# Performance work log

Hardware: AMD Instinct MI355X
Metric: run time of the kernel (lower is better)

## Reference

```python
import jax, jax.numpy as jnp
import numpy as np

N = 100_000   # nodes per type
E = 800_000   # edges per relation
H = 128       # hidden_channels
O = 64        # out_channels
TIME_SCALE = 1.0
LN_EPS = 1e-5


def setup_inputs() -> dict:
    key = jax.random.key(0)
    ks = jax.random.split(key, 24)
    nrm = lambda k, shp, s=1.0: jax.random.normal(k, shp, jnp.float32) * s
    inp = {}
    inp["x_A"] = nrm(ks[0], (N, H))
    inp["x_B"] = nrm(ks[1], (N, H))
    inp["x_C"] = nrm(ks[2], (N, H))
    inp["t_A"] = jax.random.uniform(ks[3], (N,), jnp.float32) * 1000.0
    inp["t_B"] = jax.random.uniform(ks[4], (N,), jnp.float32) * 1000.0
    inp["t_C"] = jax.random.uniform(ks[5], (N,), jnp.float32) * 1000.0
    inp["edge1"] = jnp.stack([jax.random.randint(ks[6], (E,), 0, N),
                              jax.random.randint(ks[7], (E,), 0, N)]).astype(jnp.int32)
    inp["edge2"] = jnp.stack([jax.random.randint(ks[8], (E,), 0, N),
                              jax.random.randint(ks[9], (E,), 0, N)]).astype(jnp.int32)
    kk = 10
    for i in range(2):
        inp[f"Wl{i}"] = nrm(ks[kk], (H, H), 0.05); kk += 1
        inp[f"bl{i}"] = jnp.zeros((H,), jnp.float32)
        inp[f"W0{i}"] = nrm(ks[kk], (H, H), 0.05); kk += 1
        inp[f"b0{i}"] = jnp.zeros((H,), jnp.float32)
        inp[f"W1{i}"] = nrm(ks[kk], (H, H), 0.05); kk += 1
        inp[f"b1{i}"] = jnp.zeros((H,), jnp.float32)
        inp[f"gate{i}"] = jnp.asarray(0.5, jnp.float32)
        inp[f"lam{i}"] = jnp.asarray(0.1, jnp.float32)  # raw lambda
        inp[f"lng{i}"] = jnp.ones((H,), jnp.float32)
        inp[f"lnb{i}"] = jnp.zeros((H,), jnp.float32)
    inp["Wout"] = nrm(ks[kk], (H, O), 0.05)
    inp["bout"] = jnp.zeros((O,), jnp.float32)
    return inp


def _layer(h_src, h_dst, x0_dst, edge, t_src, t_dst,
           Wl, bl, W0, b0, W1, b1, gate, raw_lam, lng, lnb):
    s, d = edge[0], edge[1]
    n_dst = h_dst.shape[0]
    # per-edge time-decay weight
    lam = jax.nn.softplus(raw_lam) + 1e-8
    delta = jnp.maximum((t_dst[d] - t_src[s]) / TIME_SCALE, 0.0)
    w = jnp.exp(jnp.maximum(-lam * delta, -60.0))          # [E]
    # gather + weight + scatter-add  (propagate with aggr='add')
    msg = h_src[s] * w[:, None]                            # [E,H]
    agg = jax.ops.segment_sum(msg, d, num_segments=n_dst)  # [n_dst,H]
    deg = jnp.maximum(jax.ops.segment_sum(w, d, num_segments=n_dst), 1e-6)
    out = agg / deg[:, None]
    g = jax.nn.sigmoid(gate)
    y = out @ Wl + bl + (1.0 - g) * (h_dst @ W0 + b0) + g * (x0_dst @ W1 + b1)
    y = jax.nn.relu(y)
    mu = jnp.mean(y, axis=-1, keepdims=True)
    var = jnp.mean((y - mu) ** 2, axis=-1, keepdims=True)
    y = (y - mu) * jax.lax.rsqrt(var + LN_EPS) * lng + lnb
    # index_copy_: only nodes that appear as a destination get updated
    cnt = jax.ops.segment_sum(jnp.ones_like(w), d, num_segments=n_dst)
    return jnp.where((cnt > 0)[:, None], y, h_dst)


def reference(x_A, x_B, x_C, t_A, t_B, t_C, edge1, edge2,
              Wl0, bl0, W00, b00, W10, b10, gate0, lam0, lng0, lnb0,
              Wl1, bl1, W01, b01, W11, b11, gate1, lam1, lng1, lnb1,
              Wout, bout):
    # reversed(metapath): process (B,r2,C) with conv_idx=1 first, then (A,r1,B) with conv_idx=0
    h_C = _layer(x_B, x_C, x_C, edge2, t_B, t_C,
                 Wl1, bl1, W01, b01, W11, b11, gate1, lam1, lng1, lnb1)
    h_B = _layer(x_A, x_B, x_B, edge1, t_A, t_B,
                 Wl0, bl0, W00, b00, W10, b10, gate0, lam0, lng0, lnb0)
    del h_B  # target type is metapath[-1][2] == 'C'; B's update does not feed C
    return h_C @ Wout + bout
```

## Files before the change

kernel.cpp:

```cpp
#include <hip/hip_runtime.h>


#define HD 128
#define OD 64
#define SCAN_E 1024

typedef unsigned short u16;
typedef short v8s __attribute__((ext_vector_type(8)));
typedef float v4f __attribute__((ext_vector_type(4)));

union Frag {
    unsigned int u[4];
    uint4 q;
    v8s v;
    u16 h[8];
};

__device__ __forceinline__ float softplus_f(float x) {
    return fmaxf(x, 0.0f) + log1pf(expf(-fabsf(x)));
}
__device__ __forceinline__ float sigmoid_f(float x) {
    return 1.0f / (1.0f + expf(-x));
}
__device__ __forceinline__ int swz(int r, int c) {
    int g = (c >> 2) ^ (r & 7);
    return r * 128 + g * 4 + (c & 3);
}

__device__ __forceinline__ void gload_lds16(const void* g, void* l) {
    __builtin_amdgcn_global_load_lds(
        (const __attribute__((address_space(1))) void*)g,
        (__attribute__((address_space(3))) void*)l, 16, 0, 0);
}

__device__ __forceinline__ void split_store(float x, u16* ph, u16* pl) {
    unsigned int b = __float_as_uint(x);
    unsigned int h = b & 0xffff0000u;
    *ph = (u16)(h >> 16);
    float r = x - __uint_as_float(h);
    *pl = (u16)(__float_as_uint(r) >> 16);
}

__device__ __forceinline__ void split_pack8(const float* f, Frag* hi, Frag* lo) {
#pragma unroll
    for (int j = 0; j < 8; ++j) {
        unsigned int b = __float_as_uint(f[j]);
        unsigned int h = b & 0xffff0000u;
        hi->h[j] = (u16)(h >> 16);
        float r = f[j] - __uint_as_float(h);
        lo->h[j] = (u16)(__float_as_uint(r) >> 16);
    }
}

__device__ __forceinline__ void cvt_split8(const float* f, unsigned int* hi,
                                           unsigned int* lo) {
#pragma unroll
    for (int j = 0; j < 4; ++j) {
        unsigned int b0 = __float_as_uint(f[2 * j]);
        unsigned int b1 = __float_as_uint(f[2 * j + 1]);
        unsigned int h0 = b0 & 0xffff0000u;
        unsigned int h1 = b1 & 0xffff0000u;
        hi[j] = (h0 >> 16) | h1;
        float r0 = f[2 * j]     - __uint_as_float(h0);
        float r1 = f[2 * j + 1] - __uint_as_float(h1);
        lo[j] = (__float_as_uint(r0) >> 16) | (__float_as_uint(r1) & 0xffff0000u);
    }
}

__device__ __forceinline__ void stage_chunk(
    const u16* __restrict__ Ah, const u16* __restrict__ Al,
    int kc, char* buf, int row0w, int lane, int N)
{
    const int rfrag = lane & 15;
    const int kb    = lane >> 4;
#pragma unroll
    for (int rt = 0; rt < 2; ++rt) {
        int rG = row0w + rt * 16 + rfrag;
        rG = (rG < N) ? rG : (N - 1);
        size_t so = (size_t)rG * HD + kc * 32 + kb * 8;
        gload_lds16(Ah + so, buf + rt * 1024);
        gload_lds16(Al + so, buf + 2048 + rt * 1024);
    }
}

__global__ __launch_bounds__(256) void k_prep(
    const int* __restrict__ edge, int* __restrict__ cnt, int E, int gE,
    const float* __restrict__ Wl, const float* __restrict__ W0,
    const float* __restrict__ W1, const float* __restrict__ Wout,
    const float* __restrict__ bl, const float* __restrict__ b0,
    const float* __restrict__ b1, const float* __restrict__ gatep,
    const float* __restrict__ xC,
    u16* __restrict__ wlh, u16* __restrict__ wll,
    u16* __restrict__ wch, u16* __restrict__ wcl,
    u16* __restrict__ woh, u16* __restrict__ wol, float* __restrict__ bc,
    u16* __restrict__ xch, u16* __restrict__ xcl, int N)
{
    if (blockIdx.x < (unsigned)gE) {
        int e = blockIdx.x * 256 + threadIdx.x;
        if (e < E) atomicAdd(cnt + edge[E + e], 1);
        return;
    }
    if (blockIdx.x < (unsigned)(gE + 97)) {
        int i = (blockIdx.x - gE) * 256 + threadIdx.x;
        const float g = sigmoid_f(gatep[0]);
        if (i < 16384) {
            int n = i >> 7, k = i & 127;
            float a  = Wl[k * 128 + n];
            float w0 = W0[k * 128 + n];
            float w1 = W1[k * 128 + n];
            float c  = (1.f - g) * w0 + g * w1;
            int off = ((k >> 5) * 128 + n) * 32 + (k & 31);
            split_store(a, wlh + off, wll + off);
            split_store(c, wch + off, wcl + off);
        } else if (i < 24576) {
            int j = i - 16384;
            int n = j >> 7, k = j & 127;
            float v = Wout[k * 64 + n];
            int off = ((k >> 5) * 64 + n) * 32 + (k & 31);
            split_store(v, woh + off, wol + off);
        } else if (i < 24704) {
            int t = i - 24576;
            bc[t] = bl[t] + (1.f - g) * b0[t] + g * b1[t];
        }
        return;
    }
    long long e8 = ((long long)(blockIdx.x - gE - 97) * 256 + threadIdx.x) * 8;
    if (e8 < (long long)N * HD) {
        float4 u0 = *reinterpret_cast<const float4*>(xC + e8);
        float4 u1 = *reinterpret_cast<const float4*>(xC + e8 + 4);
        float f[8] = {u0.x, u0.y, u0.z, u0.w, u1.x, u1.y, u1.z, u1.w};
        Frag hi, lo;
        split_pack8(f, &hi, &lo);
        *reinterpret_cast<uint4*>(xch + e8) = hi.q;
        *reinterpret_cast<uint4*>(xcl + e8) = lo.q;
    }
}

__global__ __launch_bounds__(256) void k_scan1(
    const int* __restrict__ cnt, int* __restrict__ offs,
    int* __restrict__ part, int* __restrict__ tot, int N)
{
    __shared__ int sh[256];
    const int t = threadIdx.x;
    const int base = blockIdx.x * SCAN_E + t * 4;
    int v[4], sum = 0;
#pragma unroll
    for (int i = 0; i < 4; ++i) {
        int idx = base + i;
        v[i] = (idx < N) ? cnt[idx] : 0;
        sum += v[i];
    }
    sh[t] = sum;
    __syncthreads();
    for (int off = 1; off < 256; off <<= 1) {
        int x = (t >= off) ? sh[t - off] : 0;
        __syncthreads();
        sh[t] += x;
        __syncthreads();
    }
    int run = (t > 0) ? sh[t - 1] : 0;
    if (t == 255) part[blockIdx.x] = atomicAdd(tot, sh[255]);
#pragma unroll
    for (int i = 0; i < 4; ++i) {
        int idx = base + i;
        if (idx < N) offs[idx] = run;
        run += v[i];
    }
}

__global__ __launch_bounds__(256) void k_fillw(
    const int* __restrict__ edge, const float* __restrict__ tB,
    const float* __restrict__ tC, const float* __restrict__ lam_raw,
    const int* __restrict__ offs, const int* __restrict__ part,
    int* __restrict__ fillc, int2* __restrict__ srcw, int E)
{
    int e = blockIdx.x * 256 + threadIdx.x;
    if (e >= E) return;
    int s = edge[e];
    int d = edge[E + e];
    float lam = softplus_f(lam_raw[0]) + 1e-8f;
    float dt  = fmaxf(tC[d] - tB[s], 0.0f);
    float w   = expf(fmaxf(-lam * dt, -60.0f));
    int pos = offs[d] + part[d >> 10] + atomicAdd(fillc + d, 1);
    srcw[pos] = make_int2(s, __float_as_int(w));
}

__global__ __launch_bounds__(256) void k_gather(
    const float* __restrict__ xB, const int2* __restrict__ srcw,
    const int* __restrict__ offs, const int* __restrict__ part,
    const int* __restrict__ cnt, u16* __restrict__ aggh,
    u16* __restrict__ aggl, int N)
{
    const int wave = (blockIdx.x * 256 + threadIdx.x) >> 6;
    const int lane = threadIdx.x & 63;
    const int slot = lane >> 4;
    const int l4   = lane & 15;
    if (wave >= N) return;
    const int r    = wave;
    const int degc = cnt[r];

    if (degc == 0) {
        if (slot == 0) {
            uint4 z = make_uint4(0, 0, 0, 0);
            *reinterpret_cast<uint4*>(aggh + (size_t)r * HD + l4 * 8) = z;
            *reinterpret_cast<uint4*>(aggl + (size_t)r * HD + l4 * 8) = z;
        }
        return;
    }

    const int start = offs[r] + part[r >> 10];
    float4 a0 = make_float4(0, 0, 0, 0), a1 = make_float4(0, 0, 0, 0);
    float sw = 0.f;
#pragma unroll 2
    for (int j = slot; j < degc; j += 4) {
        int2 swp = srcw[start + j];
        float w = __int_as_float(swp.y);
        const float* row = xB + (size_t)swp.x * HD + l4 * 8;
        float4 x0 = *reinterpret_cast<const float4*>(row);
        float4 x1 = *reinterpret_cast<const float4*>(row + 4);
        a0.x = fmaf(w, x0.x, a0.x); a0.y = fmaf(w, x0.y, a0.y);
        a0.z = fmaf(w, x0.z, a0.z); a0.w = fmaf(w, x0.w, a0.w);
        a1.x = fmaf(w, x1.x, a1.x); a1.y = fmaf(w, x1.y, a1.y);
        a1.z = fmaf(w, x1.z, a1.z); a1.w = fmaf(w, x1.w, a1.w);
        sw += w;
    }
#pragma unroll
    for (int m = 16; m <= 32; m <<= 1) {
        a0.x += __shfl_xor(a0.x, m); a0.y += __shfl_xor(a0.y, m);
        a0.z += __shfl_xor(a0.z, m); a0.w += __shfl_xor(a0.w, m);
        a1.x += __shfl_xor(a1.x, m); a1.y += __shfl_xor(a1.y, m);
        a1.z += __shfl_xor(a1.z, m); a1.w += __shfl_xor(a1.w, m);
        sw   += __shfl_xor(sw, m);
    }
    float inv = 1.0f / fmaxf(sw, 1e-6f);
    if (slot == 0) {
        float f[8] = {a0.x * inv, a0.y * inv, a0.z * inv, a0.w * inv,
                      a1.x * inv, a1.y * inv, a1.z * inv, a1.w * inv};
        Frag hi, lo;
        split_pack8(f, &hi, &lo);
        *reinterpret_cast<uint4*>(aggh + (size_t)r * HD + l4 * 8) = hi.q;
        *reinterpret_cast<uint4*>(aggl + (size_t)r * HD + l4 * 8) = lo.q;
    }
}

__global__ __launch_bounds__(256) void k_fused(
    const u16* __restrict__ aggh, const u16* __restrict__ aggl,
    const u16* __restrict__ xch, const u16* __restrict__ xcl,
    const float* __restrict__ xC, const int* __restrict__ cnt,
    const u16* __restrict__ wlh, const u16* __restrict__ wll,
    const u16* __restrict__ wch, const u16* __restrict__ wcl,
    const u16* __restrict__ woh, const u16* __restrict__ wol,
    const float* __restrict__ bc, const float* __restrict__ lng,
    const float* __restrict__ lnb, const float* __restrict__ bout,
    float* __restrict__ out, int N)
{
    __shared__ char lds[32768];

    const int lane = threadIdx.x & 63;
    const int wid  = threadIdx.x >> 6;
    const int lr   = lane & 15;
    const int kb   = lane >> 4;
    const int row0 = blockIdx.x * 128 + wid * 32;
    char* myb = lds + wid * 8192;
    char* bufs[2] = {myb, myb + 4096};

    const u16* Ahp[2] = {aggh, xch};
    const u16* Alp[2] = {aggl, xcl};

    v4f acc[2][8] = {};

    stage_chunk(Ahp[0], Alp[0], 0, bufs[0], row0, lane, N);
    stage_chunk(Ahp[0], Alp[0], 1, bufs[1], row0, lane, N);

#pragma unroll
    for (int ch = 0; ch < 8; ++ch) {
        const int mat = ch >> 2, kc = ch & 3;
        if (ch == 7) {
            asm volatile("s_waitcnt vmcnt(0)" ::: "memory");
        } else {
            asm volatile("s_waitcnt vmcnt(4)" ::: "memory");
        }
        const char* cb = bufs[ch & 1];

        Frag ah[2], al[2];
#pragma unroll
        for (int rt = 0; rt < 2; ++rt) {
            ah[rt].q = *reinterpret_cast<const uint4*>(cb + rt * 1024 + lane * 16);
            al[rt].q = *reinterpret_cast<const uint4*>(cb + 2048 + rt * 1024 + lane * 16);
        }
        asm volatile("s_waitcnt lgkmcnt(0)" ::: "memory");
        __builtin_amdgcn_sched_barrier(0);

        if (ch + 2 < 8) {
            const int nc = ch + 2;
            stage_chunk(Ahp[nc >> 2], Alp[nc >> 2], nc & 3,
                        bufs[ch & 1], row0, lane, N);
        }

        const uint4* BH = (const uint4*)(mat ? wch : wlh);
        const uint4* BL = (const uint4*)(mat ? wcl : wll);
#pragma unroll
        for (int ct = 0; ct < 8; ++ct) {
            int idx = kc * 512 + (ct * 16 + lr) * 4 + kb;
            Frag bh, bl;
            bh.q = BH[idx];
            bl.q = BL[idx];
#pragma unroll
            for (int rt = 0; rt < 2; ++rt) {
                acc[rt][ct] = __builtin_amdgcn_mfma_f32_16x16x32_bf16(
                    ah[rt].v, bh.v, acc[rt][ct], 0, 0, 0);
                acc[rt][ct] = __builtin_amdgcn_mfma_f32_16x16x32_bf16(
                    ah[rt].v, bl.v, acc[rt][ct], 0, 0, 0);
                acc[rt][ct] = __builtin_amdgcn_mfma_f32_16x16x32_bf16(
                    al[rt].v, bh.v, acc[rt][ct], 0, 0, 0);
            }
        }
    }

    float bcv[8], gav[8], bev[8];
#pragma unroll
    for (int ct = 0; ct < 8; ++ct) {
        int c = ct * 16 + lr;
        bcv[ct] = bc[c];
        gav[ct] = lng[c];
        bev[ct] = lnb[c];
    }
    float bov[4];
#pragma unroll
    for (int ct = 0; ct < 4; ++ct) bov[ct] = bout[ct * 16 + lr];

    const uint4* BH3 = (const uint4*)woh;
    const uint4* BL3 = (const uint4*)wol;
    float* hc = (float*)myb;

#pragma unroll
    for (int rt = 0; rt < 2; ++rt) {
        int rq = row0 + rt * 16 + kb * 4;
        int cvr[4] = {0, 0, 0, 0};
        if (rq < N) {
            int4 cv = *(const int4*)(cnt + rq);
            cvr[0] = cv.x; cvr[1] = cv.y; cvr[2] = cv.z; cvr[3] = cv.w;
        }
#pragma unroll
        for (int reg = 0; reg < 4; ++reg) {
            int rloc = kb * 4 + reg;
            int r    = rq + reg;
            float yv[8];
            float s = 0.f, q = 0.f;
#pragma unroll
            for (int ct = 0; ct < 8; ++ct) {
                float v = acc[rt][ct][reg] + bcv[ct];
                v = fmaxf(v, 0.0f);
                yv[ct] = v;
                s += v;
                q += v * v;
            }
#pragma unroll
            for (int m = 1; m < 16; m <<= 1) {
                s += __shfl_xor(s, m);
                q += __shfl_xor(q, m);
            }
            float mu   = s * (1.0f / 128.0f);
            float var  = q * (1.0f / 128.0f) - mu * mu;
            float rstd = rsqrtf(var + 1e-5f);

            if (r < N) {
                if (cvr[reg] > 0) {
#pragma unroll
                    for (int ct = 0; ct < 8; ++ct)
                        hc[swz(rloc, ct * 16 + lr)] =
                            (yv[ct] - mu) * rstd * gav[ct] + bev[ct];
                } else {
                    size_t base = (size_t)r * HD;
#pragma unroll
                    for (int ct = 0; ct < 8; ++ct)
                        hc[swz(rloc, ct * 16 + lr)] = xC[base + ct * 16 + lr];
                }
            } else {
#pragma unroll
                for (int ct = 0; ct < 8; ++ct)
                    hc[swz(rloc, ct * 16 + lr)] = 0.0f;
            }
        }

        v4f acc2[4] = {};
#pragma unroll
        for (int kc = 0; kc < 4; ++kc) {
            Frag ah, al;
            {
                int c0 = kc * 32 + kb * 8;
                float4 u0 = *reinterpret_cast<const float4*>(&hc[swz(lr, c0)]);
                float4 u1 = *reinterpret_cast<const float4*>(&hc[swz(lr, c0 + 4)]);
                float f[8] = {u0.x, u0.y, u0.z, u0.w, u1.x, u1.y, u1.z, u1.w};
                cvt_split8(f, ah.u, al.u);
            }
#pragma unroll
            for (int ct = 0; ct < 4; ++ct) {
                int idx = kc * 256 + (ct * 16 + lr) * 4 + kb;
                Frag bh, bl;
                bh.q = BH3[idx];
                bl.q = BL3[idx];
                acc2[ct] = __builtin_amdgcn_mfma_f32_16x16x32_bf16(
                    ah.v, bh.v, acc2[ct], 0, 0, 0);
                acc2[ct] = __builtin_amdgcn_mfma_f32_16x16x32_bf16(
                    ah.v, bl.v, acc2[ct], 0, 0, 0);
                acc2[ct] = __builtin_amdgcn_mfma_f32_16x16x32_bf16(
                    al.v, bh.v, acc2[ct], 0, 0, 0);
            }
        }

#pragma unroll
        for (int reg = 0; reg < 4; ++reg) {
            int r = rq + reg;
            if (r < N) {
#pragma unroll
                for (int ct = 0; ct < 4; ++ct)
                    out[(size_t)r * OD + ct * 16 + lr] = acc2[ct][reg] + bov[ct];
            }
        }
    }
}

extern "C" void kernel_launch(void* const* d_in, const int* in_sizes, int n_in,
                              void* d_out, int out_size, void* d_ws, size_t ws_size,
                              hipStream_t stream) {
    const float* xB    = (const float*)d_in[1];
    const float* xC    = (const float*)d_in[2];
    const float* tB    = (const float*)d_in[4];
    const float* tC    = (const float*)d_in[5];
    const int*   edge2 = (const int*)d_in[7];
    const float* Wl1   = (const float*)d_in[18];
    const float* bl1   = (const float*)d_in[19];
    const float* W01   = (const float*)d_in[20];
    const float* b01   = (const float*)d_in[21];
    const float* W11   = (const float*)d_in[22];
    const float* b11   = (const float*)d_in[23];
    const float* gate1 = (const float*)d_in[24];
    const float* lam1  = (const float*)d_in[25];
    const float* lng1  = (const float*)d_in[26];
    const float* lnb1  = (const float*)d_in[27];
    const float* Wout  = (const float*)d_in[28];
    const float* bout  = (const float*)d_in[29];

    const int N = in_sizes[2] / HD;
    const int E = in_sizes[7] / 2;

    int*   cnt   = (int*)d_ws;
    int*   fillc = cnt + N;
    int*   offs  = fillc + N;
    int*   part  = offs + N;
    int*   tot   = part + 128;
    int2*  srcw  = (int2*)(tot + 4);
    u16*   wlh   = (u16*)(srcw + E);
    u16*   wll   = wlh + 16384;
    u16*   wch   = wll + 16384;
    u16*   wcl   = wch + 16384;
    u16*   woh   = wcl + 16384;
    u16*   wol   = woh + 8192;
    float* bc    = (float*)(wol + 8192);
    u16*   aggh  = (u16*)(bc + 128);
    u16*   aggl  = aggh + (size_t)N * HD;
    u16*   xch   = aggl + (size_t)N * HD;
    u16*   xcl   = xch + (size_t)N * HD;

    hipMemsetAsync(cnt, 0, (size_t)2 * N * sizeof(int), stream);
    hipMemsetAsync(tot, 0, sizeof(int), stream);

    dim3 blk(256);
    const int gE = (E + 255) / 256;
    const int NB = (N + SCAN_E - 1) / SCAN_E;
    const int gX = (N * (HD / 8) + 255) / 256;

    k_prep <<<gE + 97 + gX, blk, 0, stream>>>(edge2, cnt, E, gE,
                                              Wl1, W01, W11, Wout, bl1, b01, b11,
                                              gate1, xC, wlh, wll, wch, wcl,
                                              woh, wol, bc, xch, xcl, N);
    k_scan1<<<NB, blk, 0, stream>>>(cnt, offs, part, tot, N);
    k_fillw<<<gE, blk, 0, stream>>>(edge2, tB, tC, lam1, offs, part, fillc, srcw, E);

    const int gN64 = (N * 64 + 255) / 256;
    k_gather<<<gN64, blk, 0, stream>>>(xB, srcw, offs, part, cnt, aggh, aggl, N);

    const int GB = (N + 127) / 128;
    k_fused<<<GB, blk, 0, stream>>>(aggh, aggl, xch, xcl, xC, cnt,
                                    wlh, wll, wch, wcl, woh, wol,
                                    bc, lng1, lnb1, bout, (float*)d_out, N);
}
```

Baseline: 240.0 us.

## Stage GEMM weights through shared LDS and skip negligible-weight edges in gather

The fused GEMM kernel now loads the Wl/Wc weight chunks cooperatively into LDS, double-buffered next to the activation tiles, and also stages the output projection weights in LDS, instead of having every wave read them from global memory. This adds block-wide barriers and raises LDS use to 64KB per block, which may reduce occupancy. Separately, the fill kernel records a per-destination max edge weight with atomicMax, and gather skips edges whose weight is below 1e-8 of that max, avoiding row loads that barely affect the normalized sum. The skip is an approximation that introduces a small numerical deviation. It adds an extra atomic per edge and a third N-sized memset.

```diff
diff --git a/kernel.cpp b/kernel.cpp
--- a/kernel.cpp
+++ b/kernel.cpp
@@ -67,7 +67,7 @@
     }
 }
 
-__device__ __forceinline__ void stage_chunk(
+__device__ __forceinline__ void stage_A(
     const u16* __restrict__ Ah, const u16* __restrict__ Al,
     int kc, char* buf, int row0w, int lane, int N)
 {
@@ -80,6 +80,20 @@
         size_t so = (size_t)rG * HD + kc * 32 + kb * 8;
         gload_lds16(Ah + so, buf + rt * 1024);
         gload_lds16(Al + so, buf + 2048 + rt * 1024);
+    }
+}
+
+__device__ __forceinline__ void stage_B(
+    const u16* __restrict__ Bh, const u16* __restrict__ Bl,
+    int kc, char* bbuf, int wid, int lane)
+{
+#pragma unroll
+    for (int i = 0; i < 2; ++i) {
+        int seg = wid * 2 + i;
+        gload_lds16((const char*)Bh + kc * 8192 + seg * 1024 + lane * 16,
+                    bbuf + seg * 1024);
+        gload_lds16((const char*)Bl + kc * 8192 + seg * 1024 + lane * 16,
+                    bbuf + 8192 + seg * 1024);
     }
 }
 
@@ -172,7 +186,8 @@
     const int* __restrict__ edge, const float* __restrict__ tB,
     const float* __restrict__ tC, const float* __restrict__ lam_raw,
     const int* __restrict__ offs, const int* __restrict__ part,
-    int* __restrict__ fillc, int2* __restrict__ srcw, int E)
+    int* __restrict__ fillc, int* __restrict__ wmax,
+    int2* __restrict__ srcw, int E)
 {
     int e = blockIdx.x * 256 + threadIdx.x;
     if (e >= E) return;
@@ -183,13 +198,14 @@
     float w   = expf(fmaxf(-lam * dt, -60.0f));
     int pos = offs[d] + part[d >> 10] + atomicAdd(fillc + d, 1);
     srcw[pos] = make_int2(s, __float_as_int(w));
+    atomicMax(wmax + d, __float_as_int(w));
 }
 
 __global__ __launch_bounds__(256) void k_gather(
     const float* __restrict__ xB, const int2* __restrict__ srcw,
     const int* __restrict__ offs, const int* __restrict__ part,
-    const int* __restrict__ cnt, u16* __restrict__ aggh,
-    u16* __restrict__ aggl, int N)
+    const int* __restrict__ cnt, const int* __restrict__ wmax,
+    u16* __restrict__ aggh, u16* __restrict__ aggl, int N)
 {
     const int wave = (blockIdx.x * 256 + threadIdx.x) >> 6;
     const int lane = threadIdx.x & 63;
@@ -209,12 +225,14 @@
     }
 
     const int start = offs[r] + part[r >> 10];
+    const float thr = __int_as_float(wmax[r]) * 1e-8f;
     float4 a0 = make_float4(0, 0, 0, 0), a1 = make_float4(0, 0, 0, 0);
     float sw = 0.f;
 #pragma unroll 2
     for (int j = slot; j < degc; j += 4) {
         int2 swp = srcw[start + j];
         float w = __int_as_float(swp.y);
+        if (w < thr) continue;
         const float* row = xB + (size_t)swp.x * HD + l4 * 8;
         float4 x0 = *reinterpret_cast<const float4*>(row);
         float4 x1 = *reinterpret_cast<const float4*>(row + 4);
@@ -254,67 +272,86 @@
     const float* __restrict__ lnb, const float* __restrict__ bout,
     float* __restrict__ out, int N)
 {
-    __shared__ char lds[32768];
+    __shared__ char lds[65536];
 
     const int lane = threadIdx.x & 63;
     const int wid  = threadIdx.x >> 6;
     const int lr   = lane & 15;
     const int kb   = lane >> 4;
     const int row0 = blockIdx.x * 128 + wid * 32;
-    char* myb = lds + wid * 8192;
-    char* bufs[2] = {myb, myb + 4096};
+    char* myA = lds + wid * 8192;
+    char* abufs[2] = {myA, myA + 4096};
+    char* bbufs[2] = {lds + 32768, lds + 32768 + 16384};
 
     const u16* Ahp[2] = {aggh, xch};
     const u16* Alp[2] = {aggl, xcl};
+    const u16* Bhp[2] = {wlh, wch};
+    const u16* Blp[2] = {wll, wcl};
 
     v4f acc[2][8] = {};
 
-    stage_chunk(Ahp[0], Alp[0], 0, bufs[0], row0, lane, N);
-    stage_chunk(Ahp[0], Alp[0], 1, bufs[1], row0, lane, N);
+    stage_A(Ahp[0], Alp[0], 0, abufs[0], row0, lane, N);
+    stage_B(Bhp[0], Blp[0], 0, bbufs[0], wid, lane);
+    stage_A(Ahp[0], Alp[0], 1, abufs[1], row0, lane, N);
+    stage_B(Bhp[0], Blp[0], 1, bbufs[1], wid, lane);
 
 #pragma unroll
     for (int ch = 0; ch < 8; ++ch) {
-        const int mat = ch >> 2, kc = ch & 3;
+        const int mat = ch >> 2;
         if (ch == 7) {
             asm volatile("s_waitcnt vmcnt(0)" ::: "memory");
         } else {
-            asm volatile("s_waitcnt vmcnt(4)" ::: "memory");
-        }
-        const char* cb = bufs[ch & 1];
+            asm volatile("s_waitcnt vmcnt(8)" ::: "memory");
+        }
+        __builtin_amdgcn_s_barrier();
+
+        const char* ca = abufs[ch & 1];
+        const char* cb = bbufs[ch & 1];
 
         Frag ah[2], al[2];
 #pragma unroll
         for (int rt = 0; rt < 2; ++rt) {
-            ah[rt].q = *reinterpret_cast<const uint4*>(cb + rt * 1024 + lane * 16);
-            al[rt].q = *reinterpret_cast<const uint4*>(cb + 2048 + rt * 1024 + lane * 16);
+            ah[rt].q = *reinterpret_cast<const uint4*>(ca + rt * 1024 + lane * 16);
+            al[rt].q = *reinterpret_cast<const uint4*>(ca + 2048 + rt * 1024 + lane * 16);
+        }
+        Frag bh[8], bl[8];
+#pragma unroll
+        for (int ct = 0; ct < 8; ++ct) {
+            int bo = (((ct * 16 + lr) * 4 + kb) << 4);
+            bh[ct].q = *reinterpret_cast<const uint4*>(cb + bo);
+            bl[ct].q = *reinterpret_cast<const uint4*>(cb + 8192 + bo);
         }
         asm volatile("s_waitcnt lgkmcnt(0)" ::: "memory");
         __builtin_amdgcn_sched_barrier(0);
+        __builtin_amdgcn_s_barrier();
 
         if (ch + 2 < 8) {
             const int nc = ch + 2;
-            stage_chunk(Ahp[nc >> 2], Alp[nc >> 2], nc & 3,
-                        bufs[ch & 1], row0, lane, N);
-        }
-
-        const uint4* BH = (const uint4*)(mat ? wch : wlh);
-        const uint4* BL = (const uint4*)(mat ? wcl : wll);
+            stage_A(Ahp[nc >> 2], Alp[nc >> 2], nc & 3, abufs[ch & 1], row0, lane, N);
+            stage_B(Bhp[nc >> 2], Blp[nc >> 2], nc & 3, bbufs[ch & 1], wid, lane);
+        }
+
 #pragma unroll
         for (int ct = 0; ct < 8; ++ct) {
-            int idx = kc * 512 + (ct * 16 + lr) * 4 + kb;
-            Frag bh, bl;
-            bh.q = BH[idx];
-            bl.q = BL[idx];
 #pragma unroll
             for (int rt = 0; rt < 2; ++rt) {
                 acc[rt][ct] = __builtin_amdgcn_mfma_f32_16x16x32_bf16(
-                    ah[rt].v, bh.v, acc[rt][ct], 0, 0, 0);
+                    ah[rt].v, bh[ct].v, acc[rt][ct], 0, 0, 0);
                 acc[rt][ct] = __builtin_amdgcn_mfma_f32_16x16x32_bf16(
-                    ah[rt].v, bl.v, acc[rt][ct], 0, 0, 0);
+                    ah[rt].v, bl[ct].v, acc[rt][ct], 0, 0, 0);
                 acc[rt][ct] = __builtin_amdgcn_mfma_f32_16x16x32_bf16(
-                    al[rt].v, bh.v, acc[rt][ct], 0, 0, 0);
-            }
-        }
+                    al[rt].v, bh[ct].v, acc[rt][ct], 0, 0, 0);
+            }
+        }
+        (void)mat;
+    }
+
+    __builtin_amdgcn_s_barrier();
+#pragma unroll
+    for (int i = 0; i < 8; ++i) {
+        int seg = wid * 8 + i;
+        gload_lds16((const char*)woh + seg * 1024 + lane * 16,
+                    lds + 32768 + seg * 1024);
     }
 
     float bcv[8], gav[8], bev[8];
@@ -329,9 +366,8 @@
 #pragma unroll
     for (int ct = 0; ct < 4; ++ct) bov[ct] = bout[ct * 16 + lr];
 
-    const uint4* BH3 = (const uint4*)woh;
-    const uint4* BL3 = (const uint4*)wol;
-    float* hc = (float*)myb;
+    float* hc = (float*)myA;
+    bool b3ready = false;
 
 #pragma unroll
     for (int rt = 0; rt < 2; ++rt) {
@@ -381,6 +417,12 @@
                 for (int ct = 0; ct < 8; ++ct)
                     hc[swz(rloc, ct * 16 + lr)] = 0.0f;
             }
+        }
+
+        if (!b3ready) {
+            asm volatile("s_waitcnt vmcnt(0)" ::: "memory");
+            __builtin_amdgcn_s_barrier();
+            b3ready = true;
         }
 
         v4f acc2[4] = {};
@@ -396,16 +438,16 @@
             }
 #pragma unroll
             for (int ct = 0; ct < 4; ++ct) {
-                int idx = kc * 256 + (ct * 16 + lr) * 4 + kb;
-                Frag bh, bl;
-                bh.q = BH3[idx];
-                bl.q = BL3[idx];
+                int bo = ((kc * 256 + (ct * 16 + lr) * 4 + kb) << 4);
+                Frag b3h, b3l;
+                b3h.q = *reinterpret_cast<const uint4*>(lds + 32768 + bo);
+                b3l.q = *reinterpret_cast<const uint4*>(lds + 49152 + bo);
                 acc2[ct] = __builtin_amdgcn_mfma_f32_16x16x32_bf16(
-                    ah.v, bh.v, acc2[ct], 0, 0, 0);
+                    ah.v, b3h.v, acc2[ct], 0, 0, 0);
                 acc2[ct] = __builtin_amdgcn_mfma_f32_16x16x32_bf16(
-                    ah.v, bl.v, acc2[ct], 0, 0, 0);
+                    ah.v, b3l.v, acc2[ct], 0, 0, 0);
                 acc2[ct] = __builtin_amdgcn_mfma_f32_16x16x32_bf16(
-                    al.v, bh.v, acc2[ct], 0, 0, 0);
+                    al.v, b3h.v, acc2[ct], 0, 0, 0);
             }
         }
 
@@ -447,7 +489,8 @@
 
     int*   cnt   = (int*)d_ws;
     int*   fillc = cnt + N;
-    int*   offs  = fillc + N;
+    int*   wmax  = fillc + N;
+    int*   offs  = wmax + N;
     int*   part  = offs + N;
     int*   tot   = part + 128;
     int2*  srcw  = (int2*)(tot + 4);
@@ -463,7 +506,7 @@
     u16*   xch   = aggl + (size_t)N * HD;
     u16*   xcl   = xch + (size_t)N * HD;
 
-    hipMemsetAsync(cnt, 0, (size_t)2 * N * sizeof(int), stream);
+    hipMemsetAsync(cnt, 0, (size_t)3 * N * sizeof(int), stream);
     hipMemsetAsync(tot, 0, sizeof(int), stream);
 
     dim3 blk(256);
@@ -476,10 +519,12 @@
                                               gate1, xC, wlh, wll, wch, wcl,
                                               woh, wol, bc, xch, xcl, N);
     k_scan1<<<NB, blk, 0, stream>>>(cnt, offs, part, tot, N);
-    k_fillw<<<gE, blk, 0, stream>>>(edge2, tB, tC, lam1, offs, part, fillc, srcw, E);
+    k_fillw<<<gE, blk, 0, stream>>>(edge2, tB, tC, lam1, offs, part, fillc,
+                                    wmax, srcw, E);
 
     const int gN64 = (N * 64 + 255) / 256;
-    k_gather<<<gN64, blk, 0, stream>>>(xB, srcw, offs, part, cnt, aggh, aggl, N);
+    k_gather<<<gN64, blk, 0, stream>>>(xB, srcw, offs, part, cnt, wmax,
+                                       aggh, aggl, N);
 
     const int GB = (N + 127) / 128;
     k_fused<<<GB, blk, 0, stream>>>(aggh, aggl, xch, xcl, xC, cnt,
```

After: 238.0 us. No clear change (-0.8%).
